# Kernel optimization log

Measured on AMD Instinct MI355X. Metric: run time of the kernel, lower is better.

## Reference

```python
import jax, jax.numpy as jnp
import numpy as np

N = 10000
DIM = 64
F_CONST = 1.0
B_CONST = 0.1
R_CONST = 0.01


def setup_inputs() -> dict:
    key = jax.random.key(0)
    k1, k2 = jax.random.split(key)
    t = jnp.zeros((1,), dtype=jnp.float32)  # autonomous system; t unused
    x = jax.random.uniform(k1, (N, DIM), dtype=jnp.float32)
    A = jax.random.uniform(k2, (N, N), dtype=jnp.float32)
    return {"t": t, "x": x, "A": A}


def reference(t, x, A):
    # dx/dt = f - b*x - diag(A @ (r * x x^T)).reshape(-1, 1)
    # diag(A @ x x^T)_i = sum_j A_ij <x_j, x_i> = <x_i, (A @ x)_i>
    # so the interaction term is r * rowsum(x * (A @ x)) -- same math, no NxN intermediate.
    Ax = A @ x                                        # [N, DIM]
    outer = R_CONST * jnp.sum(x * Ax, axis=1, keepdims=True)  # [N, 1]
    return F_CONST - B_CONST * x - outer              # [N, DIM] via broadcast
```

## Files before the change

### kernel.cpp

```cpp
#include <hip/hip_runtime.h>
#include <stdint.h>


#define N_ROWS 10000
#define DIM 64
#define KTILE 32
#define NKT 313
#define F_CONST 1.0f
#define B_CONST 0.1f
#define R_CONST 0.01f

typedef __attribute__((ext_vector_type(8))) short s16x8;
typedef __attribute__((ext_vector_type(4))) float f32x4;
typedef __attribute__((ext_vector_type(4))) uint32_t u32x4;

__device__ __forceinline__ uint32_t pack_bf16(float a, float b) {
    uint32_t ua = __builtin_bit_cast(uint32_t, a);
    uint32_t ub = __builtin_bit_cast(uint32_t, b);
    ua += 0x7FFFu + ((ua >> 16) & 1u);
    ub += 0x7FFFu + ((ub >> 16) & 1u);
    return (ua >> 16) | (ub & 0xFFFF0000u);
}

__global__ __launch_bounds__(256) void pack_x_kernel(const float* __restrict__ x,
                                                     uint32_t* __restrict__ ws) {
    int id = blockIdx.x * 256 + threadIdx.x;
    int frag = id >> 6;
    int L = id & 63;
    int t = frag >> 2;
    int c = frag & 3;
    int k0 = t * KTILE + (L >> 4) * 8;
    int col = c * 16 + (L & 15);
    float v[8];
#pragma unroll
    for (int j = 0; j < 8; ++j) {
        int k = k0 + j;
        v[j] = (k < N_ROWS) ? x[k * DIM + col] : 0.0f;
    }
    u32x4 p;
    p.x = pack_bf16(v[0], v[1]);
    p.y = pack_bf16(v[2], v[3]);
    p.z = pack_bf16(v[4], v[5]);
    p.w = pack_bf16(v[6], v[7]);
    ((u32x4*)ws)[id] = p;
}

__global__ __launch_bounds__(256, 4) void gemm_diffuse_kernel(
    const float* __restrict__ A, const float* __restrict__ x,
    const uint32_t* __restrict__ ws, float* __restrict__ out) {
    __shared__ float red[4][16][DIM];

    int tid = threadIdx.x;
    int w = tid >> 6;
    int L = tid & 63;
    int quad = L >> 4;
    int m = L & 15;
    int rbase = blockIdx.x * 16;
    const float* Arow = A + (size_t)(rbase + m) * N_ROWS;

    f32x4 acc[4] = {{0.f, 0.f, 0.f, 0.f},
                    {0.f, 0.f, 0.f, 0.f},
                    {0.f, 0.f, 0.f, 0.f},
                    {0.f, 0.f, 0.f, 0.f}};

    for (int t = w; t < NKT; t += 4) {
        int kg = t * KTILE + quad * 8;
        int ks = (kg < N_ROWS) ? kg : 0;
        f32x4 a0 = __builtin_nontemporal_load((const f32x4*)(Arow + ks));
        f32x4 a1 = __builtin_nontemporal_load(((const f32x4*)(Arow + ks)) + 1);
        u32x4 pa;
        pa.x = pack_bf16(a0.x, a0.y);
        pa.y = pack_bf16(a0.z, a0.w);
        pa.z = pack_bf16(a1.x, a1.y);
        pa.w = pack_bf16(a1.z, a1.w);
        s16x8 afrag = __builtin_bit_cast(s16x8, pa);

        const u32x4* pb = (const u32x4*)ws + (size_t)(t * 4) * 64 + L;
#pragma unroll
        for (int c = 0; c < 4; ++c) {
            s16x8 bfrag = __builtin_bit_cast(s16x8, pb[c * 64]);
            acc[c] = __builtin_amdgcn_mfma_f32_16x16x32_bf16(afrag, bfrag, acc[c], 0, 0, 0);
        }
    }

#pragma unroll
    for (int c = 0; c < 4; ++c)
#pragma unroll
        for (int r = 0; r < 4; ++r)
            red[w][quad * 4 + r][c * 16 + m] = acc[c][r];
    __syncthreads();

    int row = tid >> 4;
    int q = tid & 15;
    int grow = rbase + row;
    f32x4 xv = *(const f32x4*)(x + (size_t)grow * DIM + q * 4);
    f32x4 axv;
#pragma unroll
    for (int j = 0; j < 4; ++j)
        axv[j] = red[0][row][q * 4 + j] + red[1][row][q * 4 + j] +
                 red[2][row][q * 4 + j] + red[3][row][q * 4 + j];
    float partial = xv.x * axv[0] + xv.y * axv[1] + xv.z * axv[2] + xv.w * axv[3];
    partial += __shfl_xor(partial, 1);
    partial += __shfl_xor(partial, 2);
    partial += __shfl_xor(partial, 4);
    partial += __shfl_xor(partial, 8);
    float s = R_CONST * partial;

    f32x4 o;
    o.x = F_CONST - B_CONST * xv.x - s;
    o.y = F_CONST - B_CONST * xv.y - s;
    o.z = F_CONST - B_CONST * xv.z - s;
    o.w = F_CONST - B_CONST * xv.w - s;
    *(f32x4*)(out + (size_t)grow * DIM + q * 4) = o;
}

extern "C" void kernel_launch(void* const* d_in, const int* in_sizes, int n_in,
                              void* d_out, int out_size, void* d_ws, size_t ws_size,
                              hipStream_t stream) {
    const float* x = (const float*)d_in[1];
    const float* A = (const float*)d_in[2];
    float* out = (float*)d_out;
    uint32_t* ws = (uint32_t*)d_ws;

    pack_x_kernel<<<313, 256, 0, stream>>>(x, ws);
    gemm_diffuse_kernel<<<625, 256, 0, stream>>>(A, x, ws, out);
}
```

Baseline: 596.7 us.

## Split K across four blocks per row tile with atomic dot accumulation

Splits the K dimension of the A@x GEMM across four blocks per 16-row tile, raising the grid from 625 to 2500 blocks so more A-streaming work is in flight. Each block folds its partial Ax with x in registers via shuffles and atomically adds the per-row scalar into a workspace buffer, which replaces the shared-memory cross-wave reduction. A separate finalize kernel then writes the broadcast output. The cost is an extra launch, atomics, and a non-deterministic floating-point summation order.

```diff
diff --git a/kernel.cpp b/kernel.cpp
--- a/kernel.cpp
+++ b/kernel.cpp
@@ -9,6 +9,8 @@
 #define F_CONST 1.0f
 #define B_CONST 0.1f
 #define R_CONST 0.01f
+
+#define SACC_OFF_BYTES 1310720
 
 typedef __attribute__((ext_vector_type(8))) short s16x8;
 typedef __attribute__((ext_vector_type(4))) float f32x4;
@@ -23,8 +25,10 @@
 }
 
 __global__ __launch_bounds__(256) void pack_x_kernel(const float* __restrict__ x,
-                                                     uint32_t* __restrict__ ws) {
+                                                     uint32_t* __restrict__ ws,
+                                                     float* __restrict__ sacc) {
     int id = blockIdx.x * 256 + threadIdx.x;
+    if (id < N_ROWS) sacc[id] = 0.0f;
     int frag = id >> 6;
     int L = id & 63;
     int t = frag >> 2;
@@ -45,17 +49,18 @@
     ((u32x4*)ws)[id] = p;
 }
 
-__global__ __launch_bounds__(256, 4) void gemm_diffuse_kernel(
+__global__ __launch_bounds__(256, 4) void gemm_dot_kernel(
     const float* __restrict__ A, const float* __restrict__ x,
-    const uint32_t* __restrict__ ws, float* __restrict__ out) {
-    __shared__ float red[4][16][DIM];
-
+    const uint32_t* __restrict__ ws, float* __restrict__ sacc) {
     int tid = threadIdx.x;
     int w = tid >> 6;
     int L = tid & 63;
     int quad = L >> 4;
     int m = L & 15;
     int rbase = blockIdx.x * 16;
+    int q = blockIdx.y;
+    int t0 = q * 79;
+    int t1 = (q == 3) ? NKT : (t0 + 79);
     const float* Arow = A + (size_t)(rbase + m) * N_ROWS;
 
     f32x4 acc[4] = {{0.f, 0.f, 0.f, 0.f},
@@ -63,19 +68,18 @@
                     {0.f, 0.f, 0.f, 0.f},
                     {0.f, 0.f, 0.f, 0.f}};
 
-    for (int t = w; t < NKT; t += 4) {
+    for (int t = t0 + w; t < t1; t += 4) {
         int kg = t * KTILE + quad * 8;
         int ks = (kg < N_ROWS) ? kg : 0;
         f32x4 a0 = __builtin_nontemporal_load((const f32x4*)(Arow + ks));
         f32x4 a1 = __builtin_nontemporal_load(((const f32x4*)(Arow + ks)) + 1);
+        const u32x4* pb = (const u32x4*)ws + (size_t)(t * 4) * 64 + L;
         u32x4 pa;
         pa.x = pack_bf16(a0.x, a0.y);
         pa.y = pack_bf16(a0.z, a0.w);
         pa.z = pack_bf16(a1.x, a1.y);
         pa.w = pack_bf16(a1.z, a1.w);
         s16x8 afrag = __builtin_bit_cast(s16x8, pa);
-
-        const u32x4* pb = (const u32x4*)ws + (size_t)(t * 4) * 64 + L;
 #pragma unroll
         for (int c = 0; c < 4; ++c) {
             s16x8 bfrag = __builtin_bit_cast(s16x8, pb[c * 64]);
@@ -83,35 +87,37 @@
         }
     }
 
+    float p[4];
 #pragma unroll
-    for (int c = 0; c < 4; ++c)
+    for (int r = 0; r < 4; ++r) {
+        int grow = rbase + quad * 4 + r;
+        const float* xr = x + (size_t)grow * DIM + m;
+        p[r] = acc[0][r] * xr[0] + acc[1][r] * xr[16] +
+               acc[2][r] * xr[32] + acc[3][r] * xr[48];
+        p[r] += __shfl_xor(p[r], 1);
+        p[r] += __shfl_xor(p[r], 2);
+        p[r] += __shfl_xor(p[r], 4);
+        p[r] += __shfl_xor(p[r], 8);
+    }
+    if (m == 0) {
 #pragma unroll
         for (int r = 0; r < 4; ++r)
-            red[w][quad * 4 + r][c * 16 + m] = acc[c][r];
-    __syncthreads();
+            atomicAdd(&sacc[rbase + quad * 4 + r], p[r]);
+    }
+}
 
-    int row = tid >> 4;
-    int q = tid & 15;
-    int grow = rbase + row;
-    f32x4 xv = *(const f32x4*)(x + (size_t)grow * DIM + q * 4);
-    f32x4 axv;
-#pragma unroll
-    for (int j = 0; j < 4; ++j)
-        axv[j] = red[0][row][q * 4 + j] + red[1][row][q * 4 + j] +
-                 red[2][row][q * 4 + j] + red[3][row][q * 4 + j];
-    float partial = xv.x * axv[0] + xv.y * axv[1] + xv.z * axv[2] + xv.w * axv[3];
-    partial += __shfl_xor(partial, 1);
-    partial += __shfl_xor(partial, 2);
-    partial += __shfl_xor(partial, 4);
-    partial += __shfl_xor(partial, 8);
-    float s = R_CONST * partial;
-
+__global__ __launch_bounds__(256) void finalize_kernel(const float* __restrict__ x,
+                                                       const float* __restrict__ sacc,
+                                                       float* __restrict__ out) {
+    int id = blockIdx.x * 256 + threadIdx.x;
+    f32x4 xv = ((const f32x4*)x)[id];
+    float s = R_CONST * sacc[id >> 4];
     f32x4 o;
     o.x = F_CONST - B_CONST * xv.x - s;
     o.y = F_CONST - B_CONST * xv.y - s;
     o.z = F_CONST - B_CONST * xv.z - s;
     o.w = F_CONST - B_CONST * xv.w - s;
-    *(f32x4*)(out + (size_t)grow * DIM + q * 4) = o;
+    ((f32x4*)out)[id] = o;
 }
 
 extern "C" void kernel_launch(void* const* d_in, const int* in_sizes, int n_in,
@@ -121,7 +127,9 @@
     const float* A = (const float*)d_in[2];
     float* out = (float*)d_out;
     uint32_t* ws = (uint32_t*)d_ws;
+    float* sacc = (float*)((char*)d_ws + SACC_OFF_BYTES);
 
-    pack_x_kernel<<<313, 256, 0, stream>>>(x, ws);
-    gemm_diffuse_kernel<<<625, 256, 0, stream>>>(A, x, ws, out);
+    pack_x_kernel<<<313, 256, 0, stream>>>(x, ws, sacc);
+    gemm_dot_kernel<<<dim3(625, 4), 256, 0, stream>>>(A, x, ws, sacc);
+    finalize_kernel<<<625, 256, 0, stream>>>(x, sacc, out);
 }
```

Measured after the change: 586.6 us. About the same (-1.7%).
